# Optimization experiments

Hardware: AMD Instinct MI355X
Metric: run time of the kernel (lower is better)

The kernel has to match this reference:

```python
import jax, jax.numpy as jnp
import numpy as np

D_MODEL = 2048
NUM_HEADS = 16
D_Q = 1536
D_KV = 512
BS, SL = 2, 2048


def _lin(x, w, b):
    # torch nn.Linear: y = x @ w.T + b, w: [out, in]
    return jnp.einsum('...i,oi->...o', x, w) + b


def _freqs(seq_len, dim, theta=10000.0):
    # Faithful to source incl. precedence quirk: tn = 1 / ((theta ** arange) / dim).
    # float32 overflow -> inf -> tn = 0 for large exponents (identity rotation).
    exps = jnp.arange(0, dim, 2, dtype=jnp.float32)
    tn = 1.0 / ((theta ** exps) / dim)
    m = jnp.arange(seq_len, dtype=jnp.float32)
    ang = jnp.outer(m, tn)  # [sl, dim/2]
    return jnp.cos(ang), jnp.sin(ang)


def _rope(x, cos, sin):
    # x: [bs, sl, dim]; complex pairs are (x[..., 2i], x[..., 2i+1])
    xe = x[..., 0::2]
    xo = x[..., 1::2]
    re = xe * cos - xo * sin
    im = xe * sin + xo * cos
    return jnp.stack([re, im], axis=-1).reshape(x.shape)


def _init_linear(key, out_f, in_f):
    k1, k2 = jax.random.split(key)
    bound = 1.0 / np.sqrt(in_f)
    w = jax.random.uniform(k1, (out_f, in_f), jnp.float32, -bound, bound)
    b = jax.random.uniform(k2, (out_f,), jnp.float32, -bound, bound)
    return w, b


def setup_inputs() -> dict:
    key = jax.random.key(0)
    ks = jax.random.split(key, 9)
    x = jax.random.normal(ks[0], (BS, SL, D_MODEL), jnp.float32)
    w_down_q, b_down_q = _init_linear(ks[1], D_Q, D_MODEL)
    w_up_q, b_up_q = _init_linear(ks[2], D_MODEL, D_Q)
    w_down_kv, b_down_kv = _init_linear(ks[3], D_KV, D_MODEL)
    w_up_k, b_up_k = _init_linear(ks[4], D_MODEL, D_KV)
    w_up_v, b_up_v = _init_linear(ks[5], D_MODEL, D_KV)
    wq_r, bq_r = _init_linear(ks[6], D_MODEL, D_Q)
    wk_r, bk_r = _init_linear(ks[7], D_MODEL, D_KV)
    wo, bo = _init_linear(ks[8], D_MODEL, D_MODEL)
    return dict(x=x,
                w_down_q=w_down_q, b_down_q=b_down_q,
                w_up_q=w_up_q, b_up_q=b_up_q,
                w_down_kv=w_down_kv, b_down_kv=b_down_kv,
                w_up_k=w_up_k, b_up_k=b_up_k,
                w_up_v=w_up_v, b_up_v=b_up_v,
                wq_r=wq_r, bq_r=bq_r,
                wk_r=wk_r, bk_r=bk_r,
                wo=wo, bo=bo)


def reference(x, w_down_q, b_down_q, w_up_q, b_up_q, w_down_kv, b_down_kv,
              w_up_k, b_up_k, w_up_v, b_up_v, wq_r, bq_r, wk_r, bk_r, wo, bo):
    bs, sl, dim = x.shape
    nh, hd = NUM_HEADS, dim // NUM_HEADS
    cos, sin = _freqs(sl, dim)

    # Query path: down-proj -> up-proj content + decoupled RoPE branch
    ct_q = _lin(x, w_down_q, b_down_q)                       # [bs, sl, d_q]
    q_ct = _lin(ct_q, w_up_q, b_up_q)                        # [bs, sl, d_model]
    rope_q = _rope(_lin(ct_q, wq_r, bq_r), cos, sin)         # [bs, sl, d_model]
    q = (q_ct + rope_q).reshape(bs, sl, nh, hd)

    # KV path: shared latent -> separate K/V up-proj + RoPE branch on K
    ct_kv = _lin(x, w_down_kv, b_down_kv)                    # [bs, sl, d_kv]
    k_ct = _lin(ct_kv, w_up_k, b_up_k)
    rope_k = _rope(_lin(ct_kv, wk_r, bk_r), cos, sin)
    k = (k_ct + rope_k).reshape(bs, sl, nh, hd)
    v = _lin(ct_kv, w_up_v, b_up_v).reshape(bs, sl, nh, hd)

    # Attention: explicit matmul + softmax + matmul (no causal mask in source)
    scores = jnp.einsum('bqhd,bkhd->bhqk', q, k) / np.sqrt(hd)
    probs = jax.nn.softmax(scores, axis=-1)
    a = jnp.einsum('bhqk,bkhd->bqhd', probs, v).reshape(bs, sl, nh * hd)
    return _lin(a, wo, bo)
```

## Files before the change

### kernel.cpp

```cpp
#include <hip/hip_runtime.h>

typedef float f32x4 __attribute__((ext_vector_type(4)));
typedef float f32x16 __attribute__((ext_vector_type(16)));
typedef unsigned short us8 __attribute__((ext_vector_type(8)));

#define DEVINL __device__ __forceinline__

DEVINL unsigned short f2bf(float f) {
  unsigned u = __builtin_bit_cast(unsigned, f);
  u += 0x7fffu + ((u >> 16) & 1u);
  return (unsigned short)(u >> 16);
}
DEVINL float bf2f(unsigned short b) { return __builtin_bit_cast(float, ((unsigned)b) << 16); }
DEVINL us8 ld8(const unsigned short* p) { return *reinterpret_cast<const us8*>(p); }
DEVINL void mfma_bf16(f32x4& acc, us8 a, us8 b) {
  asm("v_mfma_f32_16x16x32_bf16 %0, %1, %2, %0" : "+v"(acc) : "v"(a), "v"(b));
}
DEVINL void mfma32(f32x16& acc, us8 a, us8 b) {
  asm("v_mfma_f32_32x32x16_bf16 %0, %1, %2, %0" : "+v"(acc) : "v"(a), "v"(b));
}
DEVINL unsigned cvtpk_bf16(float lo, float hi) {
  unsigned r;
  asm("v_cvt_pk_bf16_f32 %0, %1, %2" : "=v"(r) : "v"(lo), "v"(hi));
  return r;
}
DEVINL us8 us8_from4(unsigned a, unsigned b, unsigned c, unsigned d) {
  union { unsigned u[4]; us8 v; } x;
  x.u[0] = a; x.u[1] = b; x.u[2] = c; x.u[3] = d;
  return x.v;
}
DEVINL void gld16(const void* g, void* l) {
  __builtin_amdgcn_global_load_lds((const __attribute__((address_space(1))) void*)g,
                                   (__attribute__((address_space(3))) void*)l, 16, 0, 0);
}

DEVINL void cvt4(const float* __restrict__ s, unsigned short* __restrict__ d, long i) {
  float4 v = reinterpret_cast<const float4*>(s)[i];
  unsigned lo = (unsigned)f2bf(v.x) | ((unsigned)f2bf(v.y) << 16);
  unsigned hi = (unsigned)f2bf(v.z) | ((unsigned)f2bf(v.w) << 16);
  reinterpret_cast<uint2*>(d)[i] = make_uint2(lo, hi);
}

__global__ void k_prep(const float* __restrict__ x, const float* __restrict__ wdq,
                       const float* __restrict__ wdkv, const float* __restrict__ wuq,
                       const float* __restrict__ wqr, const float* __restrict__ wuk,
                       const float* __restrict__ wkr, const float* __restrict__ wuv,
                       const float* __restrict__ wo, const float* __restrict__ bdq,
                       const float* __restrict__ bdkv, const float* __restrict__ buq,
                       const float* __restrict__ bqr, const float* __restrict__ buk,
                       const float* __restrict__ bkr, const float* __restrict__ buv,
                       unsigned short* __restrict__ xb, unsigned short* __restrict__ wcd,
                       unsigned short* __restrict__ wcq, unsigned short* __restrict__ wck,
                       unsigned short* __restrict__ wob, float* __restrict__ cosT,
                       float* __restrict__ sinT, float* __restrict__ bcd,
                       float* __restrict__ bcq, float* __restrict__ bck) {
  constexpr long C0 = 2097152, C1 = C0 + 786432, C2 = C1 + 262144, C3 = C2 + 786432,
                 C4 = C3 + 786432, C5 = C4 + 262144, C6 = C5 + 262144, C7 = C6 + 262144,
                 C8 = C7 + 1048576, C9 = C8 + 2097152, C10 = C9 + 3072;
  long u = (long)blockIdx.x * 256 + threadIdx.x;
  if (u < C0) cvt4(x, xb, u);
  else if (u < C1) cvt4(wdq, wcd, u - C0);
  else if (u < C2) cvt4(wdkv, wcd + 1536L * 2048, u - C1);
  else if (u < C3) cvt4(wuq, wcq, u - C2);
  else if (u < C4) cvt4(wqr, wcq + 2048L * 1536, u - C3);
  else if (u < C5) cvt4(wuk, wck, u - C4);
  else if (u < C6) cvt4(wkr, wck + 2048L * 512, u - C5);
  else if (u < C7) cvt4(wuv, wck + 4096L * 512, u - C6);
  else if (u < C8) cvt4(wo, wob, u - C7);
  else if (u < C9) {
    long idx = u - C8;
    int s = (int)(idx >> 10), i = (int)(idx & 1023);
    float e = (float)(2 * i);
    float pw = powf(10000.0f, e);
    float tn = 1.0f / (pw / 2048.0f);
    float ang = (float)s * tn;
    cosT[idx] = cosf(ang);
    sinT[idx] = sinf(ang);
  } else if (u < C10) {
    long j4 = (u - C9) * 4;
#pragma unroll
    for (int k = 0; k < 4; ++k) {
      long j = j4 + k;
      if (j < 2048) {
        bcd[j] = j < 1536 ? bdq[j] : bdkv[j - 1536];
      } else if (j < 6144) {
        long jj = j - 2048;
        bcq[jj] = jj < 2048 ? buq[jj] : bqr[jj - 2048];
      } else {
        long jj = j - 6144;
        bck[jj] = jj < 2048 ? buk[jj] : (jj < 4096 ? bkr[jj - 2048] : buv[jj - 4096]);
      }
    }
  }
}

template <bool OUTF32>
__global__ __launch_bounds__(512) void k_gemm256(const unsigned short* __restrict__ A,
                                                 const unsigned short* __restrict__ B,
                                                 const float* __restrict__ bias,
                                                 void* __restrict__ Cout, int N, int K, int lda) {
  constexpr int SLOT = 128 * 32 + 256 * 32;
  __shared__ unsigned short lds[3 * SLOT];
  const int nwg = gridDim.x;
  const int orig = blockIdx.x;
  const int wgid = (orig & 7) * (nwg >> 3) + (orig >> 3);
  const int nbn = N >> 8;
  const int bn = wgid % nbn, bm = wgid / nbn;
  const int tid = threadIdx.x, lane = tid & 63, w = tid >> 6;
  const int g = lane >> 4, l16 = lane & 15;
  const int wm = w >> 2, wn = w & 3;
  f32x4 acc[4][4] = {};
  const unsigned short* Abase = A + (size_t)bm * 128 * lda;
  const unsigned short* Bbase = B + (size_t)bn * 256 * K;
  const int ra = tid >> 2;
  const int gca = (tid & 3) ^ ((ra >> 1) & 3);
  const int rb1 = (tid + 512) >> 2;
  const int gcb1 = ((tid + 512) & 3) ^ ((rb1 >> 1) & 3);
  const size_t aoff = (size_t)ra * lda + gca * 8;
  const size_t boff0 = (size_t)ra * K + gca * 8;
  const size_t boff1 = (size_t)rb1 * K + gcb1 * 8;
  auto STAGE = [&](int slot, int kt) {
    unsigned short* s = &lds[slot * SLOT];
    gld16(Abase + aoff + kt, s + tid * 8);
    gld16(Bbase + boff0 + kt, s + 128 * 32 + tid * 8);
    gld16(Bbase + boff1 + kt, s + 128 * 32 + (tid + 512) * 8);
  };
  const int nt = K >> 5;
  STAGE(0, 0);
  STAGE(1, 32);
  asm volatile("s_waitcnt vmcnt(3)" ::: "memory");
  asm volatile("s_barrier" ::: "memory");
  for (int t = 0; t < nt; ++t) {
    const int slot = t % 3;
    if (t + 2 < nt) STAGE((t + 2) % 3, (t + 2) * 32);
    const unsigned short* sa = &lds[slot * SLOT];
    const unsigned short* sb = sa + 128 * 32;
    us8 af[4], bf[4];
#pragma unroll
    for (int m = 0; m < 4; ++m) {
      int row = wm * 64 + m * 16 + l16;
      af[m] = ld8(&sa[row * 32 + ((g ^ ((row >> 1) & 3)) * 8)]);
    }
#pragma unroll
    for (int n = 0; n < 4; ++n) {
      int row = wn * 64 + n * 16 + l16;
      bf[n] = ld8(&sb[row * 32 + ((g ^ ((row >> 1) & 3)) * 8)]);
    }
    __builtin_amdgcn_s_setprio(1);
#pragma unroll
    for (int m = 0; m < 4; ++m)
#pragma unroll
      for (int n = 0; n < 4; ++n) mfma_bf16(acc[m][n], af[m], bf[n]);
    __builtin_amdgcn_s_setprio(0);
    if (t < nt - 2) asm volatile("s_waitcnt vmcnt(3)" ::: "memory");
    else            asm volatile("s_waitcnt vmcnt(0)" ::: "memory");
    asm volatile("s_barrier" ::: "memory");
  }
#pragma unroll
  for (int n = 0; n < 4; ++n) {
    int col = bn * 256 + wn * 64 + n * 16 + l16;
    float bv = bias[col];
#pragma unroll
    for (int m = 0; m < 4; ++m) {
      int row0 = bm * 128 + wm * 64 + m * 16 + g * 4;
#pragma unroll
      for (int r = 0; r < 4; ++r) {
        float vv = acc[m][n][r] + bv;
        if (OUTF32)
          reinterpret_cast<float*>(Cout)[(size_t)(row0 + r) * N + col] = vv;
        else
          reinterpret_cast<unsigned short*>(Cout)[(size_t)(row0 + r) * N + col] = f2bf(vv);
      }
    }
  }
}

__global__ void k_rope_combine(const unsigned short* __restrict__ src, int ldin,
                               const float* __restrict__ cosT, const float* __restrict__ sinT,
                               unsigned short* __restrict__ outp) {
  int pidx = blockIdx.x * 256 + threadIdx.x;
  if (pidx >= 4096 * 1024) return;
  int row = pidx >> 10, i = pidx & 1023;
  int s = row & 2047;
  float c = cosT[s * 1024 + i], sn = sinT[s * 1024 + i];
  const unsigned short* rp = src + (size_t)row * ldin;
  float xe = bf2f(rp[2048 + 2 * i]), xo = bf2f(rp[2048 + 2 * i + 1]);
  float re = xe * c - xo * sn;
  float im = xe * sn + xo * c;
  float q0 = bf2f(rp[2 * i]) + re;
  float q1 = bf2f(rp[2 * i + 1]) + im;
  unsigned pack = (unsigned)f2bf(q0) | ((unsigned)f2bf(q1) << 16);
  *reinterpret_cast<unsigned*>(&outp[(size_t)row * 2048 + 2 * i]) = pack;
}

__global__ __launch_bounds__(256) void k_transpose_v(const unsigned short* __restrict__ v, int ld,
                                                     unsigned short* __restrict__ vt) {
  __shared__ unsigned short t[32][33];
  int tx = threadIdx.x & 31, ty = threadIdx.x >> 5;
  int r0 = blockIdx.y * 32, c0 = blockIdx.x * 32;
#pragma unroll
  for (int jj = 0; jj < 4; ++jj)
    t[ty * 4 + jj][tx] = v[(size_t)(r0 + ty * 4 + jj) * ld + c0 + tx];
  __syncthreads();
  int b = r0 >> 11;
#pragma unroll
  for (int jj = 0; jj < 4; ++jj) {
    int colc = c0 + ty * 4 + jj;
    size_t orow = (size_t)(b * 16 + (colc >> 7)) * 128 + (colc & 127);
    vt[orow * 2048 + (r0 & 2047) + tx] = t[tx][ty * 4 + jj];
  }
}

__global__ __launch_bounds__(256, 2) void k_attn(const unsigned short* __restrict__ Qsrc,
                                                 const unsigned short* __restrict__ Kg,
                                                 const unsigned short* __restrict__ VT,
                                                 const float* __restrict__ cosT,
                                                 const float* __restrict__ sinT,
                                                 unsigned short* __restrict__ Aout) {
  __shared__ unsigned short Ks[2][64 * 128];
  __shared__ unsigned short VTs[2][128 * 64];
  const int tid = threadIdx.x, lane = tid & 63, w = tid >> 6;
  const int hh = lane >> 5, q32 = lane & 31;
  const int orig = blockIdx.x;
  const int wgid = (orig & 7) * 64 + (orig >> 3);
  const int qt = wgid & 15;
  const int hb = wgid >> 4;
  const int h = hb & 15, b = hb >> 4;
  const float SC2 = 0.08838834764831845f * 1.4426950408889634f;
  const int srow = qt * 128 + w * 32 + q32;
  us8 qf[8];
  {
    const unsigned short* Qr = Qsrc + ((size_t)b * 2048 + srow) * 4096;
#pragma unroll
    for (int ds = 0; ds < 8; ++ds) {
      int dcol = h * 128 + ds * 16 + hh * 8;
      us8 c8 = ld8(&Qr[dcol]);
      us8 r8 = ld8(&Qr[2048 + dcol]);
      unsigned wv[4];
#pragma unroll
      for (int p2 = 0; p2 < 4; ++p2) {
        int i = (dcol >> 1) + p2;
        float cc = cosT[srow * 1024 + i], ss = sinT[srow * 1024 + i];
        float xe = bf2f(r8[2 * p2]), xo = bf2f(r8[2 * p2 + 1]);
        float o0 = (bf2f(c8[2 * p2]) + xe * cc - xo * ss) * SC2;
        float o1 = (bf2f(c8[2 * p2 + 1]) + xe * ss + xo * cc) * SC2;
        wv[p2] = cvtpk_bf16(o0, o1);
      }
      qf[ds] = us8_from4(wv[0], wv[1], wv[2], wv[3]);
    }
  }
  f32x16 O[4] = {};
  float mq = -1e30f, lq = 0.f;
  const unsigned short* Kbase = Kg + (size_t)b * 2048 * 2048 + h * 128;
  const unsigned short* VTb = VT + (size_t)(b * 16 + h) * 128 * 2048;
  auto STAGE = [&](int bufi, int ktrow) {
#pragma unroll
    for (int j = 0; j < 4; ++j) {
      int ch = (j * 4 + w) * 64 + lane;
      int key = ch >> 4, cp = ch & 15;
      gld16(&Kbase[(size_t)(ktrow + key) * 2048 + (size_t)((cp ^ (key & 15)) * 8)],
            &Ks[bufi][(j * 4 + w) * 512]);
      int d = ch >> 3, c2 = ch & 7;
      gld16(&VTb[(size_t)d * 2048 + ktrow + (size_t)((c2 ^ (d & 7)) * 8)],
            &VTs[bufi][(j * 4 + w) * 512]);
    }
  };
  STAGE(0, 0);
  for (int t = 0; t < 32; ++t) {
    const int cur = t & 1;
    __syncthreads();
    if (t < 31) STAGE(cur ^ 1, (t + 1) * 64);
    f32x16 S2[2] = {};
    __builtin_amdgcn_s_setprio(1);
#pragma unroll
    for (int kb = 0; kb < 2; ++kb) {
      const int key = kb * 32 + q32;
      const int swz = key & 15;
#pragma unroll
      for (int ds = 0; ds < 8; ++ds) {
        us8 kf = ld8(&Ks[cur][key * 128 + (((ds * 2 + hh) ^ swz) * 8)]);
        mfma32(S2[kb], kf, qf[ds]);
      }
    }
    __builtin_amdgcn_s_setprio(0);
    float mx[16];
#pragma unroll
    for (int r = 0; r < 16; ++r) mx[r] = fmaxf(S2[0][r], S2[1][r]);
#pragma unroll
    for (int st = 8; st > 0; st >>= 1)
#pragma unroll
      for (int r = 0; r < st; ++r) mx[r] = fmaxf(mx[r], mx[r + st]);
    float smax = fmaxf(mx[0], __shfl_xor(mx[0], 32));
    if (!__all(smax <= mq + 8.0f)) {
      float mn = fmaxf(mq, smax);
      float fac = exp2f(mq - mn);
      lq *= fac;
      mq = mn;
#pragma unroll
      for (int r = 0; r < 16; ++r) {
        int qr = (r & 3) + 8 * (r >> 2) + 4 * hh;
        float fr = __shfl(fac, qr);
#pragma unroll
        for (int db = 0; db < 4; ++db) O[db][r] *= fr;
      }
    }
    float ps = 0.f;
    unsigned pk[2][8];
#pragma unroll
    for (int kb = 0; kb < 2; ++kb) {
      float e[16];
#pragma unroll
      for (int r = 0; r < 16; ++r) {
        e[r] = exp2f(S2[kb][r] - mq);
        ps += e[r];
      }
#pragma unroll
      for (int pp = 0; pp < 8; ++pp) pk[kb][pp] = cvtpk_bf16(e[2 * pp], e[2 * pp + 1]);
    }
    ps += __shfl_xor(ps, 32);
    lq += ps;
    __builtin_amdgcn_s_setprio(1);
#pragma unroll
    for (int ks = 0; ks < 4; ++ks) {
      const int kb = ks >> 1, kk = ks & 1;
      unsigned u_own = hh ? pk[kb][4 * kk + 2] : pk[kb][4 * kk + 0];
      unsigned v_own = hh ? pk[kb][4 * kk + 3] : pk[kb][4 * kk + 1];
      unsigned u_snd = hh ? pk[kb][4 * kk + 0] : pk[kb][4 * kk + 2];
      unsigned v_snd = hh ? pk[kb][4 * kk + 1] : pk[kb][4 * kk + 3];
      unsigned uo = (unsigned)__shfl_xor((int)u_snd, 32);
      unsigned vo = (unsigned)__shfl_xor((int)v_snd, 32);
      us8 pa = us8_from4(hh ? uo : u_own, hh ? vo : v_own, hh ? u_own : uo, hh ? v_own : vo);
#pragma unroll
      for (int db = 0; db < 4; ++db) {
        int d = db * 32 + q32;
        us8 vf = ld8(&VTs[cur][d * 64 + (((ks * 2 + hh) ^ (d & 7)) * 8)]);
        mfma32(O[db], pa, vf);
      }
    }
    __builtin_amdgcn_s_setprio(0);
  }
  float inv = 1.0f / lq;
#pragma unroll
  for (int r = 0; r < 16; ++r) {
    int qr = (r & 3) + 8 * (r >> 2) + 4 * hh;
    float ir = __shfl(inv, qr);
    size_t row = (size_t)b * 2048 + qt * 128 + w * 32 + qr;
#pragma unroll
    for (int db = 0; db < 4; ++db)
      Aout[row * 2048 + h * 128 + db * 32 + q32] = f2bf(O[db][r] * ir);
  }
}

extern "C" void kernel_launch(void* const* d_in, const int* in_sizes, int n_in, void* d_out,
                              int out_size, void* d_ws, size_t ws_size, hipStream_t stream) {
  (void)in_sizes; (void)n_in; (void)out_size; (void)ws_size;
  constexpr int Mr = 4096;
  using US = unsigned short;
  const float* x        = (const float*)d_in[0];
  const float* w_down_q = (const float*)d_in[1];
  const float* b_down_q = (const float*)d_in[2];
  const float* w_up_q   = (const float*)d_in[3];
  const float* b_up_q   = (const float*)d_in[4];
  const float* w_down_kv= (const float*)d_in[5];
  const float* b_down_kv= (const float*)d_in[6];
  const float* w_up_k   = (const float*)d_in[7];
  const float* b_up_k   = (const float*)d_in[8];
  const float* w_up_v   = (const float*)d_in[9];
  const float* b_up_v   = (const float*)d_in[10];
  const float* wq_r     = (const float*)d_in[11];
  const float* bq_r     = (const float*)d_in[12];
  const float* wk_r     = (const float*)d_in[13];
  const float* bk_r     = (const float*)d_in[14];
  const float* wo       = (const float*)d_in[15];
  const float* bo       = (const float*)d_in[16];

  char* p = (char*)d_ws;
  auto alloc = [&](size_t bytes) { char* r = p; p += (bytes + 255) & ~(size_t)255; return r; };
  float* cosT      = (float*)alloc((size_t)2048 * 1024 * 4);
  float* sinT      = (float*)alloc((size_t)2048 * 1024 * 4);
  US* wcat_kvup    = (US*)alloc((size_t)6144 * 512 * 2);
  US* wob          = (US*)alloc((size_t)2048 * 2048 * 2);
  US* ct           = (US*)alloc((size_t)Mr * 2048 * 2);
  US* t12          = (US*)alloc((size_t)Mr * 4096 * 2);
  US* vtb          = (US*)alloc((size_t)Mr * 2048 * 2);
  US* kb           = (US*)alloc((size_t)Mr * 2048 * 2);
  float* bcat_down = (float*)alloc(2048 * 4);
  float* bcat_qup  = (float*)alloc(4096 * 4);
  float* bcat_kvup = (float*)alloc(6144 * 4);
  US* xb           = (US*)alloc((size_t)Mr * 2048 * 2);
  US* wcat_down    = (US*)alloc((size_t)2048 * 2048 * 2);
  US* wcat_qup     = (US*)alloc((size_t)4096 * 1536 * 2);
  alloc((size_t)12 * 1024 * 1024);
  US* kv3  = xb;
  US* aout = ct;

  k_prep<<<dim3(33804), dim3(256), 0, stream>>>(
      x, w_down_q, w_down_kv, w_up_q, wq_r, w_up_k, wk_r, w_up_v, wo, b_down_q, b_down_kv,
      b_up_q, bq_r, b_up_k, bk_r, b_up_v, xb, wcat_down, wcat_qup, wcat_kvup, wob, cosT, sinT,
      bcat_down, bcat_qup, bcat_kvup);

  k_gemm256<false><<<dim3((2048 / 256) * (Mr / 128)), dim3(512), 0, stream>>>(
      xb, wcat_down, bcat_down, (void*)ct, 2048, 2048, 2048);
  k_gemm256<false><<<dim3((4096 / 256) * (Mr / 128)), dim3(512), 0, stream>>>(
      ct, wcat_qup, bcat_qup, (void*)t12, 4096, 1536, 2048);
  k_gemm256<false><<<dim3((6144 / 256) * (Mr / 128)), dim3(512), 0, stream>>>(
      ct + 1536, wcat_kvup, bcat_kvup, (void*)kv3, 6144, 512, 2048);
  k_rope_combine<<<dim3((4096 * 1024 + 255) / 256), dim3(256), 0, stream>>>(kv3, 6144, cosT, sinT,
                                                                            kb);
  k_transpose_v<<<dim3(64, 128), dim3(256), 0, stream>>>(kv3 + 4096, 6144, vtb);
  k_attn<<<dim3(512), dim3(256), 0, stream>>>(t12, kb, vtb, cosT, sinT, aout);
  k_gemm256<true><<<dim3((2048 / 256) * (Mr / 128)), dim3(512), 0, stream>>>(
      aout, wob, bo, d_out, 2048, 2048, 2048);
}
```

Baseline: 362.0 us.

## Use 32x32 MFMA in GEMM and enlarge attention blocks to 256 queries

The GEMM kernel switches from 16x16x32 to 32x32x16 bf16 MFMA tiles. Each wave now covers its 64x64 sub-tile with 2x2 larger accumulators and fewer LDS fragment loads per MFMA. Separately, the attention kernel moves to 512-thread blocks that handle 256 query rows each. This halves the grid and doubles how many query rows reuse each K/V tile staged in LDS. Risks are lower occupancy in attention (one block per CU requested) and a grid of only 256 blocks on a 256-CU part.

```diff
diff --git a/kernel.cpp b/kernel.cpp
--- a/kernel.cpp
+++ b/kernel.cpp
@@ -13,9 +13,6 @@
 }
 DEVINL float bf2f(unsigned short b) { return __builtin_bit_cast(float, ((unsigned)b) << 16); }
 DEVINL us8 ld8(const unsigned short* p) { return *reinterpret_cast<const us8*>(p); }
-DEVINL void mfma_bf16(f32x4& acc, us8 a, us8 b) {
-  asm("v_mfma_f32_16x16x32_bf16 %0, %1, %2, %0" : "+v"(acc) : "v"(a), "v"(b));
-}
 DEVINL void mfma32(f32x16& acc, us8 a, us8 b) {
   asm("v_mfma_f32_32x32x16_bf16 %0, %1, %2, %0" : "+v"(acc) : "v"(a), "v"(b));
 }
@@ -107,9 +104,9 @@
   const int nbn = N >> 8;
   const int bn = wgid % nbn, bm = wgid / nbn;
   const int tid = threadIdx.x, lane = tid & 63, w = tid >> 6;
-  const int g = lane >> 4, l16 = lane & 15;
+  const int r32 = lane & 31, hh = lane >> 5;
   const int wm = w >> 2, wn = w & 3;
-  f32x4 acc[4][4] = {};
+  f32x16 acc[2][2] = {};
   const unsigned short* Abase = A + (size_t)bm * 128 * lda;
   const unsigned short* Bbase = B + (size_t)bn * 256 * K;
   const int ra = tid >> 2;
@@ -135,41 +132,49 @@
     if (t + 2 < nt) STAGE((t + 2) % 3, (t + 2) * 32);
     const unsigned short* sa = &lds[slot * SLOT];
     const unsigned short* sb = sa + 128 * 32;
-    us8 af[4], bf[4];
-#pragma unroll
-    for (int m = 0; m < 4; ++m) {
-      int row = wm * 64 + m * 16 + l16;
-      af[m] = ld8(&sa[row * 32 + ((g ^ ((row >> 1) & 3)) * 8)]);
-    }
-#pragma unroll
-    for (int n = 0; n < 4; ++n) {
-      int row = wn * 64 + n * 16 + l16;
-      bf[n] = ld8(&sb[row * 32 + ((g ^ ((row >> 1) & 3)) * 8)]);
+    us8 af[2][2], bfr[2][2];
+#pragma unroll
+    for (int m2 = 0; m2 < 2; ++m2) {
+      int row = wm * 64 + m2 * 32 + r32;
+      int sw = (row >> 1) & 3;
+#pragma unroll
+      for (int s = 0; s < 2; ++s)
+        af[m2][s] = ld8(&sa[row * 32 + (((s * 2 + hh) ^ sw) * 8)]);
+    }
+#pragma unroll
+    for (int n2 = 0; n2 < 2; ++n2) {
+      int row = wn * 64 + n2 * 32 + r32;
+      int sw = (row >> 1) & 3;
+#pragma unroll
+      for (int s = 0; s < 2; ++s)
+        bfr[n2][s] = ld8(&sb[row * 32 + (((s * 2 + hh) ^ sw) * 8)]);
     }
     __builtin_amdgcn_s_setprio(1);
 #pragma unroll
-    for (int m = 0; m < 4; ++m)
-#pragma unroll
-      for (int n = 0; n < 4; ++n) mfma_bf16(acc[m][n], af[m], bf[n]);
+    for (int s = 0; s < 2; ++s)
+#pragma unroll
+      for (int m2 = 0; m2 < 2; ++m2)
+#pragma unroll
+        for (int n2 = 0; n2 < 2; ++n2) mfma32(acc[m2][n2], af[m2][s], bfr[n2][s]);
     __builtin_amdgcn_s_setprio(0);
     if (t < nt - 2) asm volatile("s_waitcnt vmcnt(3)" ::: "memory");
     else            asm volatile("s_waitcnt vmcnt(0)" ::: "memory");
     asm volatile("s_barrier" ::: "memory");
   }
 #pragma unroll
-  for (int n = 0; n < 4; ++n) {
-    int col = bn * 256 + wn * 64 + n * 16 + l16;
+  for (int n2 = 0; n2 < 2; ++n2) {
+    int col = bn * 256 + wn * 64 + n2 * 32 + r32;
     float bv = bias[col];
 #pragma unroll
-    for (int m = 0; m < 4; ++m) {
-      int row0 = bm * 128 + wm * 64 + m * 16 + g * 4;
-#pragma unroll
-      for (int r = 0; r < 4; ++r) {
-        float vv = acc[m][n][r] + bv;
+    for (int m2 = 0; m2 < 2; ++m2) {
+#pragma unroll
+      for (int r = 0; r < 16; ++r) {
+        int row = bm * 128 + wm * 64 + m2 * 32 + (r & 3) + 8 * (r >> 2) + 4 * hh;
+        float vv = acc[m2][n2][r] + bv;
         if (OUTF32)
-          reinterpret_cast<float*>(Cout)[(size_t)(row0 + r) * N + col] = vv;
+          reinterpret_cast<float*>(Cout)[(size_t)row * N + col] = vv;
         else
-          reinterpret_cast<unsigned short*>(Cout)[(size_t)(row0 + r) * N + col] = f2bf(vv);
+          reinterpret_cast<unsigned short*>(Cout)[(size_t)row * N + col] = f2bf(vv);
       }
     }
   }
@@ -211,7 +216,7 @@
   }
 }
 
-__global__ __launch_bounds__(256, 2) void k_attn(const unsigned short* __restrict__ Qsrc,
+__global__ __launch_bounds__(512, 1) void k_attn(const unsigned short* __restrict__ Qsrc,
                                                  const unsigned short* __restrict__ Kg,
                                                  const unsigned short* __restrict__ VT,
                                                  const float* __restrict__ cosT,
@@ -222,12 +227,12 @@
   const int tid = threadIdx.x, lane = tid & 63, w = tid >> 6;
   const int hh = lane >> 5, q32 = lane & 31;
   const int orig = blockIdx.x;
-  const int wgid = (orig & 7) * 64 + (orig >> 3);
-  const int qt = wgid & 15;
-  const int hb = wgid >> 4;
+  const int wgid = (orig & 7) * 32 + (orig >> 3);
+  const int qt = wgid & 7;
+  const int hb = wgid >> 3;
   const int h = hb & 15, b = hb >> 4;
   const float SC2 = 0.08838834764831845f * 1.4426950408889634f;
-  const int srow = qt * 128 + w * 32 + q32;
+  const int srow = qt * 256 + w * 32 + q32;
   us8 qf[8];
   {
     const unsigned short* Qr = Qsrc + ((size_t)b * 2048 + srow) * 4096;
@@ -255,14 +260,14 @@
   const unsigned short* VTb = VT + (size_t)(b * 16 + h) * 128 * 2048;
   auto STAGE = [&](int bufi, int ktrow) {
 #pragma unroll
-    for (int j = 0; j < 4; ++j) {
-      int ch = (j * 4 + w) * 64 + lane;
+    for (int j = 0; j < 2; ++j) {
+      int ch = (j * 8 + w) * 64 + lane;
       int key = ch >> 4, cp = ch & 15;
       gld16(&Kbase[(size_t)(ktrow + key) * 2048 + (size_t)((cp ^ (key & 15)) * 8)],
-            &Ks[bufi][(j * 4 + w) * 512]);
+            &Ks[bufi][(j * 8 + w) * 512]);
       int d = ch >> 3, c2 = ch & 7;
       gld16(&VTb[(size_t)d * 2048 + ktrow + (size_t)((c2 ^ (d & 7)) * 8)],
-            &VTs[bufi][(j * 4 + w) * 512]);
+            &VTs[bufi][(j * 8 + w) * 512]);
     }
   };
   STAGE(0, 0);
@@ -344,7 +349,7 @@
   for (int r = 0; r < 16; ++r) {
     int qr = (r & 3) + 8 * (r >> 2) + 4 * hh;
     float ir = __shfl(inv, qr);
-    size_t row = (size_t)b * 2048 + qt * 128 + w * 32 + qr;
+    size_t row = (size_t)b * 2048 + qt * 256 + w * 32 + qr;
 #pragma unroll
     for (int db = 0; db < 4; ++db)
       Aout[row * 2048 + h * 128 + db * 32 + q32] = f2bf(O[db][r] * ir);
@@ -408,7 +413,7 @@
   k_rope_combine<<<dim3((4096 * 1024 + 255) / 256), dim3(256), 0, stream>>>(kv3, 6144, cosT, sinT,
                                                                             kb);
   k_transpose_v<<<dim3(64, 128), dim3(256), 0, stream>>>(kv3 + 4096, 6144, vtb);
-  k_attn<<<dim3(512), dim3(256), 0, stream>>>(t12, kb, vtb, cosT, sinT, aout);
+  k_attn<<<dim3(256), dim3(512), 0, stream>>>(t12, kb, vtb, cosT, sinT, aout);
   k_gemm256<true><<<dim3((2048 / 256) * (Mr / 128)), dim3(512), 0, stream>>>(
       aout, wob, bo, d_out, 2048, 2048, 2048);
 }
```

Measured after the change: 375.2 us. +3.6%, slower.
